# Kernel optimization log

Hardware: AMD Instinct MI355X
Metric: run time of the kernel (lower is better)

## Reference

```python
import jax, jax.numpy as jnp
import numpy as np

TOP_K = 8
ALPHA = 0.1
EPS = 1e-20


def setup_inputs() -> dict:
    key = jax.random.key(0)
    k1, k2 = jax.random.split(key)
    B, S, D, E = 4, 8192, 1024, 64
    hidden_states = jax.random.normal(k1, (B, S, D), dtype=jnp.float32)
    # kaiming_uniform_(a=sqrt(5)) on [E, D] -> bound = 1/sqrt(D)
    bound = 1.0 / np.sqrt(D)
    W = jax.random.uniform(k2, (E, D), dtype=jnp.float32, minval=-bound, maxval=bound)
    return {"hidden_states": hidden_states, "W": W}


def reference(hidden_states, W):
    B, S, D = hidden_states.shape
    E = W.shape[0]
    x = hidden_states.reshape(-1, D)                       # [T, D], T = B*S
    logits = jnp.einsum('td,ed->te', x, W)                 # [T, E]
    scores = jax.nn.softmax(logits, axis=-1)               # [T, E]
    top_k_weights, top_k_idx = jax.lax.top_k(scores, TOP_K)  # [T, K]
    # norm_topk_experts renormalization
    top_k_weights = top_k_weights / (top_k_weights.sum(axis=-1, keepdims=True) + EPS)
    # seq_aux loss: per-batch expert selection counts via scatter-add
    idx = top_k_idx.reshape(B, -1)                         # [B, S*K]
    ce = jnp.zeros((B, E), dtype=jnp.float32).at[jnp.arange(B)[:, None], idx].add(1.0)
    mean_scores = scores.reshape(B, S, E).mean(axis=1)     # [B, E]
    aux_loss = (ce * mean_scores).sum(axis=1).mean() * ALPHA
    return top_k_idx, top_k_weights, aux_loss
```

## Files before the change

### kernel.cpp

```cpp
#include <hip/hip_runtime.h>

#define TOKS   32768
#define NEXP   64
#define DDIM   1024
#define SEQ    8192
#define NBATCH 4
#define TPB    64
#define STR    68
#define CSTR   21
#define BK     64
#define NCHK   (DDIM / BK)
#define WTILE  (NEXP * 16 * 16)

typedef __attribute__((ext_vector_type(8)))  short short8v;
typedef __attribute__((ext_vector_type(16))) float f32x16;

__device__ __forceinline__ unsigned f2bf(float x) {
  unsigned u = __float_as_uint(x);
  return (u + 0x7fffu + ((u >> 16) & 1u)) >> 16;
}
__device__ __forceinline__ float bf2f(unsigned h) { return __uint_as_float(h << 16); }

__device__ __forceinline__ void gload_lds16(const void* g, void* s) {
  __builtin_amdgcn_global_load_lds(
      (const __attribute__((address_space(1))) unsigned int*)g,
      (__attribute__((address_space(3))) unsigned int*)s, 16, 0, 0);
}

__device__ __forceinline__ void conv8(const float4 p0, const float4 p1,
                                      unsigned* h, unsigned* lo) {
  float ff[8] = {p0.x, p0.y, p0.z, p0.w, p1.x, p1.y, p1.z, p1.w};
#pragma unroll
  for (int i = 0; i < 4; ++i) {
    unsigned h0 = f2bf(ff[2 * i]), h1 = f2bf(ff[2 * i + 1]);
    h[i] = h0 | (h1 << 16);
    unsigned l0 = f2bf(ff[2 * i] - bf2f(h0));
    unsigned l1 = f2bf(ff[2 * i + 1] - bf2f(h1));
    lo[i] = l0 | (l1 << 16);
  }
}

__global__ void moe_wsplit(const float* __restrict__ W, ushort* __restrict__ W2) {
  const int sid = blockIdx.x * 256 + threadIdx.x;
  const int p  = sid & 15;
  const int e  = (sid >> 4) & 63;
  const int kc = sid >> 10;
  const int sl = p ^ (e & 15);
  const int k0 = kc * BK + (sl & 7) * 8;
  const float* src = W + (size_t)e * DDIM + k0;
  float f[8];
  *(float4*)&f[0] = *(const float4*)src;
  *(float4*)&f[4] = *(const float4*)(src + 4);
  ushort o[8];
  if (sl < 8) {
#pragma unroll
    for (int j = 0; j < 8; ++j) o[j] = (ushort)f2bf(f[j]);
  } else {
#pragma unroll
    for (int j = 0; j < 8; ++j) {
      unsigned hb = f2bf(f[j]);
      o[j] = (ushort)f2bf(f[j] - bf2f(hb));
    }
  }
  *(short8v*)(W2 + (size_t)sid * 8) = *(const short8v*)o;
}

__global__ __launch_bounds__(256, 2) void moe_gate_main(
    const float* __restrict__ X, const ushort* __restrict__ W2,
    float* __restrict__ out, float* __restrict__ gsum, float* __restrict__ gce,
    int* __restrict__ flag_cnt, int* __restrict__ flag_tok)
{
  __shared__ __align__(16) char smem[47104];

  float* xs   = (float*)smem;
  float* wsm  = (float*)(smem + 17408);
  float* red  = (float*)(smem + 34816);
  float* gmx  = (float*)(smem + 35840);
  float* cval = (float*)(smem + 36096);
  int*   cidx = (int*)  (smem + 41472);
  int*   hist = (int*)  (smem + 46848);

  const int tid = threadIdx.x;
  const int tok_base = blockIdx.x * TPB;
  const int bb = blockIdx.x >> 7;

  const int l = tid & 63, q = tid >> 6;
  const int wm = q >> 1, wn = q & 1;
  const int rr = l & 31;
  const int kh = l >> 5;

  const float* xrow = X + (size_t)(tok_base + wm * 32 + rr) * DDIM + kh * 8;
  const char* w2c = (const char*)W2;
  const int btrow = (wn * 32 + rr) * 256;
  const int bxor  = (wn * 32 + rr) & 15;

  f32x16 acc = (f32x16)0.0f;
  float4 px[8];
  unsigned aH[16], aL[16];

#pragma unroll
  for (int s = 0; s < 4; ++s) {
    px[2 * s]     = *(const float4*)(xrow + s * 16);
    px[2 * s + 1] = *(const float4*)(xrow + s * 16 + 4);
  }
#pragma unroll
  for (int i = 0; i < 4; ++i)
    gload_lds16(w2c + q * 4096 + i * 1024 + l * 16, smem + q * 4096 + i * 1024);
#pragma unroll
  for (int s = 0; s < 4; ++s) conv8(px[2 * s], px[2 * s + 1], &aH[4 * s], &aL[4 * s]);
  __syncthreads();

  int cur = 0;
#pragma unroll 1
  for (int kc = 0; kc < NCHK; ++kc) {
    if (kc + 1 < NCHK) {
      const float* xr = xrow + (kc + 1) * BK;
#pragma unroll
      for (int s = 0; s < 4; ++s) {
        px[2 * s]     = *(const float4*)(xr + s * 16);
        px[2 * s + 1] = *(const float4*)(xr + s * 16 + 4);
      }
      const char* g = w2c + (size_t)(kc + 1) * WTILE + q * 4096 + l * 16;
      char* d = smem + ((cur ^ 1) * 16384) + q * 4096;
#pragma unroll
      for (int i = 0; i < 4; ++i) gload_lds16(g + i * 1024, d + i * 1024);
    }
    const char* tb = smem + cur * 16384 + btrow;
#pragma unroll
    for (int s = 0; s < 4; ++s) {
      short8v bh = *(const short8v*)(tb + (((2 * s + kh) ^ bxor) * 16));
      short8v bl = *(const short8v*)(tb + (((8 + 2 * s + kh) ^ bxor) * 16));
      union { short8v v; unsigned u[4]; } ua, ul;
#pragma unroll
      for (int i = 0; i < 4; ++i) { ua.u[i] = aH[4 * s + i]; ul.u[i] = aL[4 * s + i]; }
      acc = __builtin_amdgcn_mfma_f32_32x32x16_bf16(ua.v, bh, acc, 0, 0, 0);
      acc = __builtin_amdgcn_mfma_f32_32x32x16_bf16(ul.v, bh, acc, 0, 0, 0);
      acc = __builtin_amdgcn_mfma_f32_32x32x16_bf16(ua.v, bl, acc, 0, 0, 0);
    }
    if (kc + 1 < NCHK) {
#pragma unroll
      for (int s = 0; s < 4; ++s) conv8(px[2 * s], px[2 * s + 1], &aH[4 * s], &aL[4 * s]);
    }
    __syncthreads();
    cur ^= 1;
  }

  {
    const int ccol = wn * 32 + rr;
#pragma unroll
    for (int r = 0; r < 16; ++r) {
      const int trow = wm * 32 + (r & 3) + 8 * (r >> 2) + 4 * kh;
      wsm[trow * STR + ccol] = acc[r];
    }
  }
  if (tid < 64) hist[tid] = 0;
  __syncthreads();

  float* logits  = wsm;
  float* scoresT = xs;
  const int t = l;

  float m = -__builtin_huge_valf();
#pragma unroll
  for (int e = 0; e < 16; ++e) m = fmaxf(m, logits[t * STR + q * 16 + e]);
  red[q * 64 + t] = m;
  __syncthreads();
  float gm = fmaxf(fmaxf(red[t], red[64 + t]), fmaxf(red[128 + t], red[192 + t]));
  if (q == 0) gmx[t] = gm;
  float z = 0.0f;
#pragma unroll
  for (int e = 0; e < 16; ++e) {
    float ev = expf(logits[t * STR + q * 16 + e] - gm);
    scoresT[(q * 16 + e) * STR + t] = ev;
    z += ev;
  }
  __syncthreads();
  red[q * 64 + t] = z;
  __syncthreads();
  float Z = red[t] + red[64 + t] + red[128 + t] + red[192 + t];
  float invZ = 1.0f / Z;
#pragma unroll
  for (int e = 0; e < 16; ++e) scoresT[(q * 16 + e) * STR + t] *= invZ;
  __syncthreads();

  {
    const int e = l, g = q;
    float s = 0.0f;
#pragma unroll
    for (int tt = 0; tt < 16; ++tt) s += scoresT[e * STR + g * 16 + tt];
    red[g * 64 + e] = s;
  }
  __syncthreads();
  if (tid < 64) {
    float tot = red[tid] + red[64 + tid] + red[128 + tid] + red[192 + tid];
    atomicAdd(&gsum[bb * 64 + tid], tot);
  }

  if (tid < 128) {
    const int h = tid >> 6;
    const int eb = h * 32;
#pragma unroll 1
    for (int k = 0; k < 9; ++k) {
      float mv = -1.0f; int mi = eb;
#pragma unroll 4
      for (int e = 0; e < 32; ++e) {
        float v = scoresT[(eb + e) * STR + t];
        if (v > mv) { mv = v; mi = eb + e; }
      }
      cval[t * CSTR + h * 9 + k] = mv;
      cidx[t * CSTR + h * 9 + k] = mi;
      scoresT[mi * STR + t] = -1.0f;
    }
  }
  __syncthreads();

  if (tid < 64) {
    float wv[9]; int wi[8];
#pragma unroll 1
    for (int k = 0; k < 9; ++k) {
      float mv = -1.0f; int mj = 0;
#pragma unroll 3
      for (int j = 0; j < 18; ++j) {
        float v = cval[t * CSTR + j];
        if (v > mv) { mv = v; mj = j; }
      }
      wv[k] = mv;
      if (k < 8) {
        wi[k] = cidx[t * CSTR + mj];
        atomicAdd(&hist[wi[k]], 1);
      }
      cval[t * CSTR + mj] = -1.0f;
    }
    bool flag = false;
#pragma unroll
    for (int k = 0; k < 8; ++k)
      if (wv[k + 1] >= wv[k] * (1.0f - 2.0e-5f)) flag = true;
    if (flag) {
      int p = atomicAdd(flag_cnt, 1);
      flag_tok[p] = tok_base + t;
    }
    double ed[8]; double den = 0.0;
#pragma unroll
    for (int k = 0; k < 8; ++k) {
      ed[k] = exp((double)logits[t * STR + wi[k]] - (double)gmx[t]);
      den += ed[k];
    }
    const size_t tg = (size_t)(tok_base + t);
    *(float4*)(out + tg * 8) =
        make_float4((float)wi[0], (float)wi[1], (float)wi[2], (float)wi[3]);
    *(float4*)(out + tg * 8 + 4) =
        make_float4((float)wi[4], (float)wi[5], (float)wi[6], (float)wi[7]);
    *(float4*)(out + (size_t)TOKS * 8 + tg * 8) =
        make_float4((float)(ed[0] / den), (float)(ed[1] / den),
                    (float)(ed[2] / den), (float)(ed[3] / den));
    *(float4*)(out + (size_t)TOKS * 8 + tg * 8 + 4) =
        make_float4((float)(ed[4] / den), (float)(ed[5] / den),
                    (float)(ed[6] / den), (float)(ed[7] / den));
  }
  __syncthreads();
  if (tid < 64) atomicAdd(&gce[bb * 64 + tid], (float)hist[tid]);
}

__global__ __launch_bounds__(256) void moe_refine(
    const float* __restrict__ X, const float* __restrict__ W,
    float* __restrict__ out, float* __restrict__ gce,
    const int* __restrict__ flag_cnt, const int* __restrict__ flag_tok)
{
  __shared__ __align__(16) float xrow[DDIM];
  __shared__ double part[4][NEXP];
  const int tid = threadIdx.x;
  const int n = *flag_cnt;
  const int e = tid & 63;
  const int c = tid >> 6;
#pragma unroll 1
  for (int it = blockIdx.x; it < n; it += 256) {
    const int tok = flag_tok[it];
    __syncthreads();
    *(float4*)&xrow[tid * 4] = *(const float4*)&X[(size_t)tok * DDIM + tid * 4];
    __syncthreads();
    const float* wr = W + (size_t)e * DDIM + c * 256;
    const float* xr = xrow + c * 256;
    double s0 = 0.0, s1 = 0.0, s2 = 0.0, s3 = 0.0;
#pragma unroll 4
    for (int j = 0; j < 256; j += 4) {
      s0 += (double)xr[j]     * (double)wr[j];
      s1 += (double)xr[j + 1] * (double)wr[j + 1];
      s2 += (double)xr[j + 2] * (double)wr[j + 2];
      s3 += (double)xr[j + 3] * (double)wr[j + 3];
    }
    part[c][e] = (s0 + s1) + (s2 + s3);
    __syncthreads();
    if (tid < 64) {
      double cur = (part[0][e] + part[1][e]) + (part[2][e] + part[3][e]);
      int wi[8]; double wl[8];
#pragma unroll 1
      for (int k = 0; k < 8; ++k) {
        double mv = cur; int mi = e;
#pragma unroll
        for (int off = 1; off < 64; off <<= 1) {
          double ov = __shfl_xor(mv, off);
          int    oi = __shfl_xor(mi, off);
          if (ov > mv || (ov == mv && oi < mi)) { mv = ov; mi = oi; }
        }
        wi[k] = mi; wl[k] = mv;
        if (e == mi) cur = -1.0e300;
      }
      if (e == 0) {
        int olde[8];
#pragma unroll
        for (int k = 0; k < 8; ++k) olde[k] = (int)out[(size_t)tok * 8 + k];
        double ex[8]; double den = 0.0;
#pragma unroll
        for (int k = 0; k < 8; ++k) { ex[k] = exp(wl[k] - wl[0]); den += ex[k]; }
#pragma unroll
        for (int k = 0; k < 8; ++k) {
          out[(size_t)tok * 8 + k] = (float)wi[k];
          out[(size_t)TOKS * 8 + (size_t)tok * 8 + k] = (float)(ex[k] / den);
        }
        const int bbb = tok >> 13;
#pragma unroll 1
        for (int k = 0; k < 8; ++k) {
          bool in_new = false, in_old = false;
          for (int j = 0; j < 8; ++j) {
            if (wi[j] == olde[k]) in_new = true;
            if (olde[j] == wi[k]) in_old = true;
          }
          if (!in_new) atomicAdd(&gce[bbb * 64 + olde[k]], -1.0f);
          if (!in_old) atomicAdd(&gce[bbb * 64 + wi[k]], 1.0f);
        }
      }
    }
  }
}

__global__ void moe_gate_aux(const float* __restrict__ gsum,
                             const float* __restrict__ gce,
                             float* __restrict__ out)
{
  __shared__ float r[256];
  const int tid = threadIdx.x;
  r[tid] = gce[tid] * gsum[tid];
  __syncthreads();
  for (int s = 128; s > 0; s >>= 1) {
    if (tid < s) r[tid] += r[tid + s];
    __syncthreads();
  }
  if (tid == 0)
    out[(size_t)TOKS * 16] = 0.1f * r[0] / ((float)SEQ * (float)NBATCH);
}

extern "C" void kernel_launch(void* const* d_in, const int* in_sizes, int n_in,
                              void* d_out, int out_size, void* d_ws, size_t ws_size,
                              hipStream_t stream)
{
  const float* X = (const float*)d_in[0];
  const float* W = (const float*)d_in[1];
  float* out  = (float*)d_out;
  float* gsum = (float*)d_ws;
  float* gce  = gsum + NBATCH * NEXP;
  int* flag_cnt = (int*)((char*)d_ws + 2048);
  int* flag_tok = (int*)((char*)d_ws + 2176);
  ushort* W2 = (ushort*)((char*)d_ws + (1 << 20));

  hipMemsetAsync(d_ws, 0, 2176, stream);
  moe_wsplit<<<64, 256, 0, stream>>>(W, W2);
  moe_gate_main<<<TOKS / TPB, 256, 0, stream>>>(X, W2, out, gsum, gce, flag_cnt, flag_tok);
  moe_refine<<<256, 256, 0, stream>>>(X, W, out, gce, flag_cnt, flag_tok);
  moe_gate_aux<<<1, 256, 0, stream>>>(gsum, gce, out);
}
```

Before: 241.1 us.

## Stage X tiles through LDS with async loads and split MFMA accumulators

Activation rows are now copied into a swizzled, double-buffered LDS tile with global_load_lds instead of going through register prefetch. Each wave reads them back from LDS and converts to hi/lo bf16 inside the MFMA loop. The MFMA chain is split across two accumulators to shorten the dependency chain. This raises LDS to 64 KB per block, which may cap occupancy at two blocks per CU. It also moves the fp32-to-bf16 conversion onto the critical path of each chunk.

```diff
diff --git a/kernel.cpp b/kernel.cpp
--- a/kernel.cpp
+++ b/kernel.cpp
@@ -10,7 +10,8 @@
 #define CSTR   21
 #define BK     64
 #define NCHK   (DDIM / BK)
-#define WTILE  (NEXP * 16 * 16)
+#define WTILE  16384
+#define XTILE  16384
 
 typedef __attribute__((ext_vector_type(8)))  short short8v;
 typedef __attribute__((ext_vector_type(16))) float f32x16;
@@ -70,7 +71,7 @@
     float* __restrict__ out, float* __restrict__ gsum, float* __restrict__ gce,
     int* __restrict__ flag_cnt, int* __restrict__ flag_tok)
 {
-  __shared__ __align__(16) char smem[47104];
+  __shared__ __align__(16) char smem[65536];
 
   float* xs   = (float*)smem;
   float* wsm  = (float*)(smem + 17408);
@@ -89,57 +90,60 @@
   const int rr = l & 31;
   const int kh = l >> 5;
 
-  const float* xrow = X + (size_t)(tok_base + wm * 32 + rr) * DDIM + kh * 8;
+  const char* Xb = (const char*)X + (size_t)tok_base * DDIM * 4;
+  int gofs[4];
+#pragma unroll
+  for (int i = 0; i < 4; ++i) {
+    const int r  = 16 * q + 4 * i + (l >> 4);
+    const int sl = (l & 15) ^ (r & 15);
+    gofs[i] = r * 4096 + sl * 16;
+  }
   const char* w2c = (const char*)W2;
-  const int btrow = (wn * 32 + rr) * 256;
-  const int bxor  = (wn * 32 + rr) & 15;
-
-  f32x16 acc = (f32x16)0.0f;
-  float4 px[8];
-  unsigned aH[16], aL[16];
-
-#pragma unroll
-  for (int s = 0; s < 4; ++s) {
-    px[2 * s]     = *(const float4*)(xrow + s * 16);
-    px[2 * s + 1] = *(const float4*)(xrow + s * 16 + 4);
-  }
+
+  const int arow = (wm * 32 + rr) * 256;
+  const int brow = (wn * 32 + rr) * 256;
+  const int rxor = rr & 15;
+
+  f32x16 accA = (f32x16)0.0f, accB = (f32x16)0.0f;
+
 #pragma unroll
   for (int i = 0; i < 4; ++i)
-    gload_lds16(w2c + q * 4096 + i * 1024 + l * 16, smem + q * 4096 + i * 1024);
-#pragma unroll
-  for (int s = 0; s < 4; ++s) conv8(px[2 * s], px[2 * s + 1], &aH[4 * s], &aL[4 * s]);
+    gload_lds16(Xb + gofs[i], smem + q * 4096 + i * 1024);
+#pragma unroll
+  for (int i = 0; i < 4; ++i)
+    gload_lds16(w2c + q * 4096 + i * 1024 + l * 16, smem + 32768 + q * 4096 + i * 1024);
   __syncthreads();
 
   int cur = 0;
 #pragma unroll 1
   for (int kc = 0; kc < NCHK; ++kc) {
     if (kc + 1 < NCHK) {
-      const float* xr = xrow + (kc + 1) * BK;
-#pragma unroll
-      for (int s = 0; s < 4; ++s) {
-        px[2 * s]     = *(const float4*)(xr + s * 16);
-        px[2 * s + 1] = *(const float4*)(xr + s * 16 + 4);
-      }
-      const char* g = w2c + (size_t)(kc + 1) * WTILE + q * 4096 + l * 16;
-      char* d = smem + ((cur ^ 1) * 16384) + q * 4096;
-#pragma unroll
-      for (int i = 0; i < 4; ++i) gload_lds16(g + i * 1024, d + i * 1024);
-    }
-    const char* tb = smem + cur * 16384 + btrow;
+      const char* xg = Xb + (kc + 1) * 256;
+      char* xd = smem + (cur ^ 1) * XTILE + q * 4096;
+#pragma unroll
+      for (int i = 0; i < 4; ++i) gload_lds16(xg + gofs[i], xd + i * 1024);
+      const char* wg = w2c + (size_t)(kc + 1) * WTILE + q * 4096 + l * 16;
+      char* wd = smem + 32768 + (cur ^ 1) * WTILE + q * 4096;
+#pragma unroll
+      for (int i = 0; i < 4; ++i) gload_lds16(wg + i * 1024, wd + i * 1024);
+    }
+    const char* ta = smem + cur * XTILE + arow;
+    const char* tb = smem + 32768 + cur * WTILE + brow;
 #pragma unroll
     for (int s = 0; s < 4; ++s) {
-      short8v bh = *(const short8v*)(tb + (((2 * s + kh) ^ bxor) * 16));
-      short8v bl = *(const short8v*)(tb + (((8 + 2 * s + kh) ^ bxor) * 16));
+      const int q0 = 4 * s + 2 * kh;
+      float4 f0 = *(const float4*)(ta + ((q0 ^ rxor) * 16));
+      float4 f1 = *(const float4*)(ta + (((q0 + 1) ^ rxor) * 16));
+      unsigned ah[4], al[4];
+      conv8(f0, f1, ah, al);
+      short8v bh = *(const short8v*)(tb + (((2 * s + kh) ^ rxor) * 16));
+      short8v bl = *(const short8v*)(tb + (((8 + 2 * s + kh) ^ rxor) * 16));
       union { short8v v; unsigned u[4]; } ua, ul;
 #pragma unroll
-      for (int i = 0; i < 4; ++i) { ua.u[i] = aH[4 * s + i]; ul.u[i] = aL[4 * s + i]; }
-      acc = __builtin_amdgcn_mfma_f32_32x32x16_bf16(ua.v, bh, acc, 0, 0, 0);
-      acc = __builtin_amdgcn_mfma_f32_32x32x16_bf16(ul.v, bh, acc, 0, 0, 0);
-      acc = __builtin_amdgcn_mfma_f32_32x32x16_bf16(ua.v, bl, acc, 0, 0, 0);
-    }
-    if (kc + 1 < NCHK) {
-#pragma unroll
-      for (int s = 0; s < 4; ++s) conv8(px[2 * s], px[2 * s + 1], &aH[4 * s], &aL[4 * s]);
+      for (int i = 0; i < 4; ++i) { ua.u[i] = ah[i]; ul.u[i] = al[i]; }
+      accA = __builtin_amdgcn_mfma_f32_32x32x16_bf16(ua.v, bh, accA, 0, 0, 0);
+      accB = __builtin_amdgcn_mfma_f32_32x32x16_bf16(ul.v, bh, accB, 0, 0, 0);
+      accA = __builtin_amdgcn_mfma_f32_32x32x16_bf16(ua.v, bl, accA, 0, 0, 0);
     }
     __syncthreads();
     cur ^= 1;
@@ -150,7 +154,7 @@
 #pragma unroll
     for (int r = 0; r < 16; ++r) {
       const int trow = wm * 32 + (r & 3) + 8 * (r >> 2) + 4 * kh;
-      wsm[trow * STR + ccol] = acc[r];
+      wsm[trow * STR + ccol] = accA[r] + accB[r];
     }
   }
   if (tid < 64) hist[tid] = 0;
```

After: 236.5 us. Within noise of the previous version (-1.9%).

## Stage X split-bf16 tiles in LDS and read W fragments directly from global

Applied to the files above, without the earlier changes.

Restructures the gating GEMM main loop. The fp32 X tile is now loaded with coalesced row-wise accesses, split into hi/lo bf16 and written to swizzled LDS. The pre-split W is repacked into an MFMA-fragment order and read straight from global/L2 instead of being staged through LDS. The K chunk doubles to 128, two accumulators break the MFMA dependency chain, and launch bounds ask for three blocks per CU. The cost is an extra barrier per iteration and W traffic now going through cache instead of async LDS loads.

```diff
diff --git a/kernel.cpp b/kernel.cpp
--- a/kernel.cpp
+++ b/kernel.cpp
@@ -8,9 +8,8 @@
 #define TPB    64
 #define STR    68
 #define CSTR   21
-#define BK     64
+#define BK     128
 #define NCHK   (DDIM / BK)
-#define WTILE  (NEXP * 16 * 16)
 
 typedef __attribute__((ext_vector_type(8)))  short short8v;
 typedef __attribute__((ext_vector_type(16))) float f32x16;
@@ -21,38 +20,19 @@
 }
 __device__ __forceinline__ float bf2f(unsigned h) { return __uint_as_float(h << 16); }
 
-__device__ __forceinline__ void gload_lds16(const void* g, void* s) {
-  __builtin_amdgcn_global_load_lds(
-      (const __attribute__((address_space(1))) unsigned int*)g,
-      (__attribute__((address_space(3))) unsigned int*)s, 16, 0, 0);
-}
-
-__device__ __forceinline__ void conv8(const float4 p0, const float4 p1,
-                                      unsigned* h, unsigned* lo) {
-  float ff[8] = {p0.x, p0.y, p0.z, p0.w, p1.x, p1.y, p1.z, p1.w};
-#pragma unroll
-  for (int i = 0; i < 4; ++i) {
-    unsigned h0 = f2bf(ff[2 * i]), h1 = f2bf(ff[2 * i + 1]);
-    h[i] = h0 | (h1 << 16);
-    unsigned l0 = f2bf(ff[2 * i] - bf2f(h0));
-    unsigned l1 = f2bf(ff[2 * i + 1] - bf2f(h1));
-    lo[i] = l0 | (l1 << 16);
-  }
-}
-
-__global__ void moe_wsplit(const float* __restrict__ W, ushort* __restrict__ W2) {
+__global__ void moe_wsplit(const float* __restrict__ W, ushort* __restrict__ W3) {
   const int sid = blockIdx.x * 256 + threadIdx.x;
-  const int p  = sid & 15;
-  const int e  = (sid >> 4) & 63;
-  const int kc = sid >> 10;
-  const int sl = p ^ (e & 15);
-  const int k0 = kc * BK + (sl & 7) * 8;
+  const int p  = sid & 3;
+  const int e  = (sid >> 2) & 63;
+  const int g  = sid >> 8;
+  const int kh = p & 1;
+  const int k0 = g * 16 + kh * 8;
   const float* src = W + (size_t)e * DDIM + k0;
   float f[8];
   *(float4*)&f[0] = *(const float4*)src;
   *(float4*)&f[4] = *(const float4*)(src + 4);
   ushort o[8];
-  if (sl < 8) {
+  if (p < 2) {
 #pragma unroll
     for (int j = 0; j < 8; ++j) o[j] = (ushort)f2bf(f[j]);
   } else {
@@ -62,11 +42,11 @@
       o[j] = (ushort)f2bf(f[j] - bf2f(hb));
     }
   }
-  *(short8v*)(W2 + (size_t)sid * 8) = *(const short8v*)o;
-}
-
-__global__ __launch_bounds__(256, 2) void moe_gate_main(
-    const float* __restrict__ X, const ushort* __restrict__ W2,
+  *(short8v*)(W3 + (size_t)sid * 8) = *(const short8v*)o;
+}
+
+__global__ __launch_bounds__(256, 3) void moe_gate_main(
+    const float* __restrict__ X, const ushort* __restrict__ W3,
     float* __restrict__ out, float* __restrict__ gsum, float* __restrict__ gce,
     int* __restrict__ flag_cnt, int* __restrict__ flag_tok)
 {
@@ -89,60 +69,80 @@
   const int rr = l & 31;
   const int kh = l >> 5;
 
-  const float* xrow = X + (size_t)(tok_base + wm * 32 + rr) * DDIM + kh * 8;
-  const char* w2c = (const char*)W2;
-  const int btrow = (wn * 32 + rr) * 256;
-  const int bxor  = (wn * 32 + rr) & 15;
-
-  f32x16 acc = (f32x16)0.0f;
+  const int xr0 = tid >> 5;
+  const int xc  = tid & 31;
+  const float* Xbase = X + (size_t)tok_base * DDIM;
+  int wb[8];
+#pragma unroll
+  for (int i = 0; i < 8; ++i) {
+    const int r = xr0 + 8 * i;
+    wb[i] = r * 256 + ((((xc >> 1) ^ (r & 15)) << 4)) + ((xc & 1) * 8);
+  }
+
+  const int abase = (wm * 32 + rr) * 256;
+  const int amask = (wm * 32 + rr) & 15;
+  const ushort* Wb = W3 + (size_t)(wn * 32 + rr) * 32 + kh * 8;
+
+  f32x16 accA = (f32x16)0.0f, accB = (f32x16)0.0f;
+
   float4 px[8];
-  unsigned aH[16], aL[16];
-
-#pragma unroll
-  for (int s = 0; s < 4; ++s) {
-    px[2 * s]     = *(const float4*)(xrow + s * 16);
-    px[2 * s + 1] = *(const float4*)(xrow + s * 16 + 4);
-  }
-#pragma unroll
-  for (int i = 0; i < 4; ++i)
-    gload_lds16(w2c + q * 4096 + i * 1024 + l * 16, smem + q * 4096 + i * 1024);
-#pragma unroll
-  for (int s = 0; s < 4; ++s) conv8(px[2 * s], px[2 * s + 1], &aH[4 * s], &aL[4 * s]);
-  __syncthreads();
-
-  int cur = 0;
+  unsigned sh[16], sl[16];
+
+#define LOADPX(kc) do { \
+    const float* xsrc = Xbase + (kc) * BK; \
+    _Pragma("unroll") \
+    for (int i = 0; i < 8; ++i) \
+      px[i] = *(const float4*)(xsrc + (size_t)(xr0 + 8 * i) * DDIM + xc * 4); \
+  } while (0)
+
+#define CONV() do { \
+    _Pragma("unroll") \
+    for (int i = 0; i < 8; ++i) { \
+      unsigned h0 = f2bf(px[i].x), h1 = f2bf(px[i].y); \
+      unsigned h2 = f2bf(px[i].z), h3 = f2bf(px[i].w); \
+      sh[2 * i]     = h0 | (h1 << 16); \
+      sh[2 * i + 1] = h2 | (h3 << 16); \
+      sl[2 * i]     = f2bf(px[i].x - bf2f(h0)) | (f2bf(px[i].y - bf2f(h1)) << 16); \
+      sl[2 * i + 1] = f2bf(px[i].z - bf2f(h2)) | (f2bf(px[i].w - bf2f(h3)) << 16); \
+    } } while (0)
+
+#define WRITE() do { \
+    _Pragma("unroll") \
+    for (int i = 0; i < 8; ++i) { \
+      *(uint2*)(smem + wb[i])         = make_uint2(sh[2 * i], sh[2 * i + 1]); \
+      *(uint2*)(smem + 16384 + wb[i]) = make_uint2(sl[2 * i], sl[2 * i + 1]); \
+    } } while (0)
+
+#define COMPUTE(kc) do { \
+    _Pragma("unroll") \
+    for (int s = 0; s < 8; ++s) { \
+      const int g = (kc) * 8 + s; \
+      const ushort* wp = Wb + (size_t)g * 2048; \
+      short8v bh = *(const short8v*)wp; \
+      short8v bl = *(const short8v*)(wp + 16); \
+      const int aoff = abase + (((2 * s + kh) ^ amask) << 4); \
+      short8v ah = *(const short8v*)(smem + aoff); \
+      short8v al = *(const short8v*)(smem + 16384 + aoff); \
+      accA = __builtin_amdgcn_mfma_f32_32x32x16_bf16(ah, bh, accA, 0, 0, 0); \
+      accB = __builtin_amdgcn_mfma_f32_32x32x16_bf16(al, bh, accB, 0, 0, 0); \
+      accA = __builtin_amdgcn_mfma_f32_32x32x16_bf16(ah, bl, accA, 0, 0, 0); \
+    } } while (0)
+
+  LOADPX(0);
+  CONV();
+  WRITE();
+  __syncthreads();
+
 #pragma unroll 1
   for (int kc = 0; kc < NCHK; ++kc) {
+    if (kc + 1 < NCHK) LOADPX(kc + 1);
+    COMPUTE(kc);
+    if (kc + 1 < NCHK) CONV();
+    __syncthreads();
     if (kc + 1 < NCHK) {
-      const float* xr = xrow + (kc + 1) * BK;
-#pragma unroll
-      for (int s = 0; s < 4; ++s) {
-        px[2 * s]     = *(const float4*)(xr + s * 16);
-        px[2 * s + 1] = *(const float4*)(xr + s * 16 + 4);
-      }
-      const char* g = w2c + (size_t)(kc + 1) * WTILE + q * 4096 + l * 16;
-      char* d = smem + ((cur ^ 1) * 16384) + q * 4096;
-#pragma unroll
-      for (int i = 0; i < 4; ++i) gload_lds16(g + i * 1024, d + i * 1024);
-    }
-    const char* tb = smem + cur * 16384 + btrow;
-#pragma unroll
-    for (int s = 0; s < 4; ++s) {
-      short8v bh = *(const short8v*)(tb + (((2 * s + kh) ^ bxor) * 16));
-      short8v bl = *(const short8v*)(tb + (((8 + 2 * s + kh) ^ bxor) * 16));
-      union { short8v v; unsigned u[4]; } ua, ul;
-#pragma unroll
-      for (int i = 0; i < 4; ++i) { ua.u[i] = aH[4 * s + i]; ul.u[i] = aL[4 * s + i]; }
-      acc = __builtin_amdgcn_mfma_f32_32x32x16_bf16(ua.v, bh, acc, 0, 0, 0);
-      acc = __builtin_amdgcn_mfma_f32_32x32x16_bf16(ul.v, bh, acc, 0, 0, 0);
-      acc = __builtin_amdgcn_mfma_f32_32x32x16_bf16(ua.v, bl, acc, 0, 0, 0);
-    }
-    if (kc + 1 < NCHK) {
-#pragma unroll
-      for (int s = 0; s < 4; ++s) conv8(px[2 * s], px[2 * s + 1], &aH[4 * s], &aL[4 * s]);
-    }
-    __syncthreads();
-    cur ^= 1;
+      WRITE();
+      __syncthreads();
+    }
   }
 
   {
@@ -150,11 +150,16 @@
 #pragma unroll
     for (int r = 0; r < 16; ++r) {
       const int trow = wm * 32 + (r & 3) + 8 * (r >> 2) + 4 * kh;
-      wsm[trow * STR + ccol] = acc[r];
+      wsm[trow * STR + ccol] = accA[r] + accB[r];
     }
   }
   if (tid < 64) hist[tid] = 0;
   __syncthreads();
+
+#undef LOADPX
+#undef CONV
+#undef WRITE
+#undef COMPUTE
 
   float* logits  = wsm;
   float* scoresT = xs;
@@ -360,11 +365,11 @@
   float* gce  = gsum + NBATCH * NEXP;
   int* flag_cnt = (int*)((char*)d_ws + 2048);
   int* flag_tok = (int*)((char*)d_ws + 2176);
-  ushort* W2 = (ushort*)((char*)d_ws + (1 << 20));
+  ushort* W3 = (ushort*)((char*)d_ws + (1 << 20));
 
   hipMemsetAsync(d_ws, 0, 2176, stream);
-  moe_wsplit<<<64, 256, 0, stream>>>(W, W2);
-  moe_gate_main<<<TOKS / TPB, 256, 0, stream>>>(X, W2, out, gsum, gce, flag_cnt, flag_tok);
+  moe_wsplit<<<64, 256, 0, stream>>>(W, W3);
+  moe_gate_main<<<TOKS / TPB, 256, 0, stream>>>(X, W3, out, gsum, gce, flag_cnt, flag_tok);
   moe_refine<<<256, 256, 0, stream>>>(X, W, out, gce, flag_cnt, flag_tok);
   moe_gate_aux<<<1, 256, 0, stream>>>(gsum, gce, out);
 }
```

After: 254.9 us. 5.7% more time.
